# Kernel optimization log

Hardware: AMD Instinct MI355X
Metric: run time of the kernel (lower is better)

The kernel has to match this reference:

```python
import jax, jax.numpy as jnp
import numpy as np

ALPHA = 0.2          # LeakyReLU negative slope
NEG_INF = -9e15      # mask fill value used by the original module


def setup_inputs() -> dict:
    key = jax.random.key(0)
    k1, k2, k3, k4 = jax.random.split(key, 4)
    N, F_in, F_out = 8192, 256, 64
    h = jax.random.normal(k1, (N, F_in), dtype=jnp.float32)
    adj = jax.random.randint(k2, (N, N), 0, 2).astype(jnp.int32)
    # xavier_uniform with gain=1.414
    gain = 1.414
    bW = gain * np.sqrt(6.0 / (F_in + F_out))
    W = jax.random.uniform(k3, (F_in, F_out), dtype=jnp.float32, minval=-bW, maxval=bW)
    ba = gain * np.sqrt(6.0 / (2 * F_out + 1))
    a = jax.random.uniform(k4, (2 * F_out, 1), dtype=jnp.float32, minval=-ba, maxval=ba)
    return {"h": h, "adj": adj, "W": W, "a": a}


def reference(h, adj, W, a):
    # Wh: [N, F_out]
    Wh = h @ W
    F_out = Wh.shape[1]
    # Decompose a_input @ a: e[i, j] = leakyrelu(Wh[j]@a[:F] + Wh[i]@a[F:])
    # (repeat gives Wh[j] in the first half, repeat_interleave gives Wh[i] in the second)
    f_src = (Wh @ a[:F_out]).reshape(-1)   # [N], coefficient of column index j
    f_dst = (Wh @ a[F_out:]).reshape(-1)   # [N], coefficient of row index i
    e = jax.nn.leaky_relu(f_dst[:, None] + f_src[None, :], negative_slope=ALPHA)  # [N, N]
    attention = jnp.where(adj > 0, e, NEG_INF)
    attention = jax.nn.softmax(attention, axis=1)
    # dropout is identity in eval mode (training=False)
    h_prime = attention @ Wh               # [N, F_out]
    return jax.nn.elu(h_prime)             # concat=True path
```

## Files before the change

### kernel.cpp

```cpp
#include <hip/hip_runtime.h>
#include <hip/hip_bf16.h>

#define GN     8192
#define FIN    256
#define FOUT   64
#define NSPLIT 8
#define JSEG   1024
#define NCH    32
#define GRP    4
#define ROWS_B 128
#define LOG2E  1.44269504f

typedef float  f32x4  __attribute__((ext_vector_type(4)));
typedef __bf16 bf16x8 __attribute__((ext_vector_type(8)));
typedef int    iv4    __attribute__((ext_vector_type(4)));

__device__ __forceinline__ unsigned short f2bf_rtne(float x) {
    unsigned int u = __float_as_uint(x);
    unsigned int r = (u + 0x7FFFu + ((u >> 16) & 1u)) >> 16;
    return (unsigned short)r;
}

__global__ __launch_bounds__(256) void k_wh(const float* __restrict__ h,
                                            const float* __restrict__ W,
                                            const float* __restrict__ a,
                                            float* __restrict__ fsrc,
                                            float* __restrict__ fdst,
                                            uint4* __restrict__ whfrag) {
    __shared__ float Wt[FOUT][FIN + 1];
    __shared__ float WhL[32][FOUT + 1];
    int t = threadIdx.x;
    int col = t & 63, kq4 = t >> 6;
#pragma unroll
    for (int rep = 0; rep < 16; ++rep) {
        int k0 = kq4 * 4 + rep * 16;
        float4 wv;
        wv.x = W[(k0 + 0) * FOUT + col];
        wv.y = W[(k0 + 1) * FOUT + col];
        wv.z = W[(k0 + 2) * FOUT + col];
        wv.w = W[(k0 + 3) * FOUT + col];
        *(float4*)&Wt[col][k0] = wv;
    }
    __syncthreads();
    int wave = t >> 6, lane = t & 63;
    float a1 = a[lane], a2 = a[FOUT + lane];
    int bid = blockIdx.x;
#pragma unroll
    for (int rr = 0; rr < 8; ++rr) {
        int il = wave * 8 + rr;
        int i  = bid * 32 + il;
        const float* hrow = h + (size_t)i * FIN;
        float acc = 0.f;
#pragma unroll 8
        for (int k0 = 0; k0 < FIN; k0 += 4) {
            float4 hv = *(const float4*)&hrow[k0];
            float4 wv = *(const float4*)&Wt[lane][k0];
            acc += hv.x * wv.x + hv.y * wv.y + hv.z * wv.z + hv.w * wv.w;
        }
        WhL[il][lane] = acc;
        float v1 = acc * a1, v2 = acc * a2;
#pragma unroll
        for (int off = 32; off > 0; off >>= 1) {
            v1 += __shfl_xor(v1, off);
            v2 += __shfl_xor(v2, off);
        }
        if (lane == 0) {
            fsrc[i] = fminf(v1, 30.f) * LOG2E;
            fdst[i] = fminf(v2, 30.f) * LOG2E;
        }
    }
    __syncthreads();
    int lane2 = t & 63, ct = t >> 6;
    int colc = ct * 16 + (lane2 & 15);
    int gb = lane2 >> 4;
    unsigned int pk[4];
#pragma unroll
    for (int p = 0; p < 4; ++p) {
        int jo = ((p >> 1) * 16) + gb * 4 + (p & 1) * 2;
        unsigned int lo = f2bf_rtne(WhL[jo    ][colc]);
        unsigned int hi = f2bf_rtne(WhL[jo + 1][colc]);
        pk[p] = lo | (hi << 16);
    }
    uint4 o; o.x = pk[0]; o.y = pk[1]; o.z = pk[2]; o.w = pk[3];
    whfrag[(size_t)(bid * 4 + ct) * 64 + lane2] = o;
}

__global__ __launch_bounds__(512, 2) void k_attn(const int* __restrict__ adj,
                                                 const float* __restrict__ fsrc,
                                                 const float* __restrict__ fdst,
                                                 const uint4* __restrict__ whfrag,
                                                 float* __restrict__ pacc,
                                                 float* __restrict__ pden) {
    __shared__ uint4 whL[NCH * 4 * 64];
    __shared__ float fsL[JSEG];
    __shared__ unsigned bbuf[8][2][16][4];

    int t = threadIdx.x, wv = t >> 6, lane = t & 63;
    int bid = blockIdx.x;
    int rt = bid >> 3, q = bid & (NSPLIT - 1);
    int rowbase = rt * ROWS_B;
    int r = lane & 15, g = lane >> 4;
    int row16 = rowbase + wv * 16;

    const int* abase = adj + (size_t)row16 * GN + q * JSEG;
    iv4 st[16];
#pragma unroll
    for (int k = 0; k < 16; ++k)
        st[k] = *(const iv4*)(abase + (size_t)k * GN + lane * 4);

    {
        const uint4* src = whfrag + (size_t)q * (NCH * 4 * 64);
#pragma unroll
        for (int it = 0; it < 16; ++it) whL[it * 512 + t] = src[it * 512 + t];
        if (t < 256) *(float4*)&fsL[t * 4] = *(const float4*)&fsrc[q * JSEG + t * 4];
    }
    __syncthreads();

    float d = fdst[row16 + r];
    f32x4 acc0 = {0.f, 0.f, 0.f, 0.f}, acc1 = acc0, acc2 = acc0, acc3 = acc0;
    float den = 0.f;

    for (int grp = 0; grp < GRP; ++grp) {
#pragma unroll
        for (int k = 0; k < 16; ++k) {
            iv4 v = st[k];
            unsigned long long b0 = __ballot(v[0] > 0);
            unsigned long long b1 = __ballot(v[1] > 0);
            unsigned long long b2 = __ballot(v[2] > 0);
            unsigned long long b3 = __ballot(v[3] > 0);
            if (lane < 8) {
                unsigned long long s01 = (lane & 1) ? b1 : b0;
                unsigned long long s23 = (lane & 1) ? b3 : b2;
                unsigned long long ss  = (lane & 2) ? s23 : s01;
                bbuf[wv][lane >> 2][k][lane & 3] = (unsigned)(ss >> ((lane >> 2) * 32));
            }
        }
        if (grp + 1 < GRP) {
#pragma unroll
            for (int k = 0; k < 16; ++k)
                st[k] = *(const iv4*)(abase + (size_t)k * GN + (grp + 1) * 256 + lane * 4);
        }
#pragma unroll 4
        for (int chl = 0; chl < 8; ++chl) {
            int ch = grp * 8 + chl;
            uint4 W4 = *(const uint4*)&bbuf[wv][chl >> 2][r][0];
            float4 s0 = *(const float4*)&fsL[ch * 32 + g * 4];
            float4 s1 = *(const float4*)&fsL[ch * 32 + 16 + g * 4];
            const uint4* bl = &whL[(ch * 4) * 64 + lane];
            uint4 b0 = bl[0], b1 = bl[64], b2 = bl[128], b3 = bl[192];
            unsigned wc[4] = {W4.x, W4.y, W4.z, W4.w};
            float se[8] = {s0.x, s0.y, s0.z, s0.w, s1.x, s1.y, s1.z, s1.w};
            int sb = (chl & 3) * 8 + g;
            bf16x8 af;
            float ws = 0.f;
#pragma unroll
            for (int e = 0; e < 8; ++e) {
                float ev = d + se[e];
                float lr = fmaxf(ev, 0.2f * ev);
                float ex = __builtin_amdgcn_exp2f(lr);
                unsigned bit = (wc[e & 3] >> (sb + (e >> 2) * 4)) & 1u;
                float wvv = bit ? ex : 0.f;
                ws += wvv;
                af[e] = (__bf16)wvv;
            }
            den += ws;
            acc0 = __builtin_amdgcn_mfma_f32_16x16x32_bf16(af, __builtin_bit_cast(bf16x8, b0), acc0, 0, 0, 0);
            acc1 = __builtin_amdgcn_mfma_f32_16x16x32_bf16(af, __builtin_bit_cast(bf16x8, b1), acc1, 0, 0, 0);
            acc2 = __builtin_amdgcn_mfma_f32_16x16x32_bf16(af, __builtin_bit_cast(bf16x8, b2), acc2, 0, 0, 0);
            acc3 = __builtin_amdgcn_mfma_f32_16x16x32_bf16(af, __builtin_bit_cast(bf16x8, b3), acc3, 0, 0, 0);
        }
    }

    den += __shfl_xor(den, 16);
    den += __shfl_xor(den, 32);

    float* po = pacc + (size_t)q * (GN * FOUT);
    int orow = rowbase + wv * 16 + g * 4;
#pragma unroll
    for (int reg = 0; reg < 4; ++reg) {
        po[(size_t)(orow + reg) * FOUT +  0 + r] = acc0[reg];
        po[(size_t)(orow + reg) * FOUT + 16 + r] = acc1[reg];
        po[(size_t)(orow + reg) * FOUT + 32 + r] = acc2[reg];
        po[(size_t)(orow + reg) * FOUT + 48 + r] = acc3[reg];
    }
    if (g == 0) pden[(size_t)q * GN + row16 + r] = den;
}

__global__ __launch_bounds__(256) void k_out(const float* __restrict__ pacc,
                                             const float* __restrict__ pden,
                                             float* __restrict__ out) {
    int idx = blockIdx.x * 256 + threadIdx.x;
    int i = idx >> 6;
    float num = 0.f, den = 0.f;
#pragma unroll
    for (int qq = 0; qq < NSPLIT; ++qq) {
        num += pacc[(size_t)qq * (GN * FOUT) + idx];
        den += pden[(size_t)qq * GN + i];
    }
    float v = (den != 0.f) ? num / den : 0.f;
    out[idx] = v > 0.f ? v : __expf(v) - 1.f;
}

extern "C" void kernel_launch(void* const* d_in, const int* in_sizes, int n_in,
                              void* d_out, int out_size, void* d_ws, size_t ws_size,
                              hipStream_t stream) {
    (void)in_sizes; (void)n_in; (void)out_size; (void)ws_size;
    const float* h   = (const float*)d_in[0];
    const int*   adj = (const int*)d_in[1];
    const float* W   = (const float*)d_in[2];
    const float* a   = (const float*)d_in[3];
    float* out = (float*)d_out;

    float* ws     = (float*)d_ws;
    float* fsrc   = ws;
    float* fdst   = fsrc + GN;
    uint4* whfrag = (uint4*)(fdst + GN);
    float* pacc   = (float*)(whfrag + (size_t)GN / 32 * 4 * 64);
    float* pden   = pacc + (size_t)NSPLIT * GN * FOUT;

    k_wh  <<<GN / 32,                 256, 0, stream>>>(h, W, a, fsrc, fdst, whfrag);
    k_attn<<<(GN / ROWS_B) * NSPLIT,  512, 0, stream>>>(adj, fsrc, fdst, whfrag, pacc, pden);
    k_out <<<GN * FOUT / 256,         256, 0, stream>>>(pacc, pden, out);
}
```

Measured before the change: 111.9 us.

## Pack adjacency into bitmask in separate streaming kernel before attention

Adds a k_pack kernel that reads the full int32 adjacency matrix with nontemporal loads, several in flight at once, and writes a compact per-row bitmask. The attention kernel then loads its mask bits straight into registers instead of ballot-packing adj through shared memory interleaved with the MFMA work. The adjacency read moves into a dedicated streaming pass, and the attention kernel loses its LDS staging and barrier-free ballot stage. The cost is an extra launch and a small bitmask write and read through global memory.

New measurement: 122.5 us. 9.5% more time.

```diff
diff --git a/kernel.cpp b/kernel.cpp
--- a/kernel.cpp
+++ b/kernel.cpp
@@ -7,7 +7,6 @@
 #define NSPLIT 8
 #define JSEG   1024
 #define NCH    32
-#define GRP    4
 #define ROWS_B 128
 #define LOG2E  1.44269504f
 
@@ -19,6 +18,34 @@
     unsigned int u = __float_as_uint(x);
     unsigned int r = (u + 0x7FFFu + ((u >> 16) & 1u)) >> 16;
     return (unsigned short)r;
+}
+
+__global__ __launch_bounds__(256) void k_pack(const int* __restrict__ adj,
+                                              unsigned* __restrict__ bmask) {
+    int wv = threadIdx.x >> 6, lane = threadIdx.x & 63;
+    int row = blockIdx.x * 4 + wv;
+    const int* rp = adj + (size_t)row * GN;
+    iv4 st[4];
+#pragma unroll
+    for (int dd = 0; dd < 4; ++dd)
+        st[dd] = __builtin_nontemporal_load((const iv4*)(rp + dd * 256 + lane * 4));
+#pragma unroll 4
+    for (int gg = 0; gg < 32; ++gg) {
+        iv4 v = st[gg & 3];
+        unsigned long long b0 = __ballot(v[0] > 0);
+        unsigned long long b1 = __ballot(v[1] > 0);
+        unsigned long long b2 = __ballot(v[2] > 0);
+        unsigned long long b3 = __ballot(v[3] > 0);
+        int ng = gg + 4;
+        if (ng < 32)
+            st[gg & 3] = __builtin_nontemporal_load((const iv4*)(rp + ng * 256 + lane * 4));
+        if (lane < 8) {
+            unsigned long long s01 = (lane & 1) ? b1 : b0;
+            unsigned long long s23 = (lane & 1) ? b3 : b2;
+            unsigned long long ss  = (lane & 2) ? s23 : s01;
+            bmask[(size_t)row * 256 + gg * 8 + lane] = (unsigned)(ss >> ((lane >> 2) * 32));
+        }
+    }
 }
 
 __global__ __launch_bounds__(256) void k_wh(const float* __restrict__ h,
@@ -85,7 +112,7 @@
     whfrag[(size_t)(bid * 4 + ct) * 64 + lane2] = o;
 }
 
-__global__ __launch_bounds__(512, 2) void k_attn(const int* __restrict__ adj,
+__global__ __launch_bounds__(512, 2) void k_attn(const unsigned* __restrict__ bmask,
                                                  const float* __restrict__ fsrc,
                                                  const float* __restrict__ fdst,
                                                  const uint4* __restrict__ whfrag,
@@ -93,20 +120,19 @@
                                                  float* __restrict__ pden) {
     __shared__ uint4 whL[NCH * 4 * 64];
     __shared__ float fsL[JSEG];
-    __shared__ unsigned bbuf[8][2][16][4];
 
     int t = threadIdx.x, wv = t >> 6, lane = t & 63;
     int bid = blockIdx.x;
     int rt = bid >> 3, q = bid & (NSPLIT - 1);
     int rowbase = rt * ROWS_B;
     int r = lane & 15, g = lane >> 4;
-    int row16 = rowbase + wv * 16;
-
-    const int* abase = adj + (size_t)row16 * GN + q * JSEG;
-    iv4 st[16];
-#pragma unroll
-    for (int k = 0; k < 16; ++k)
-        st[k] = *(const iv4*)(abase + (size_t)k * GN + lane * 4);
+    int row = rowbase + wv * 16 + r;
+
+    const uint4* bm4 = (const uint4*)bmask + (size_t)row * 64 + q * 8;
+    uint4 M[8];
+#pragma unroll
+    for (int i = 0; i < 8; ++i) M[i] = bm4[i];
+    float d = fdst[row];
 
     {
         const uint4* src = whfrag + (size_t)q * (NCH * 4 * 64);
@@ -116,34 +142,15 @@
     }
     __syncthreads();
 
-    float d = fdst[row16 + r];
     f32x4 acc0 = {0.f, 0.f, 0.f, 0.f}, acc1 = acc0, acc2 = acc0, acc3 = acc0;
     float den = 0.f;
 
-    for (int grp = 0; grp < GRP; ++grp) {
-#pragma unroll
-        for (int k = 0; k < 16; ++k) {
-            iv4 v = st[k];
-            unsigned long long b0 = __ballot(v[0] > 0);
-            unsigned long long b1 = __ballot(v[1] > 0);
-            unsigned long long b2 = __ballot(v[2] > 0);
-            unsigned long long b3 = __ballot(v[3] > 0);
-            if (lane < 8) {
-                unsigned long long s01 = (lane & 1) ? b1 : b0;
-                unsigned long long s23 = (lane & 1) ? b3 : b2;
-                unsigned long long ss  = (lane & 2) ? s23 : s01;
-                bbuf[wv][lane >> 2][k][lane & 3] = (unsigned)(ss >> ((lane >> 2) * 32));
-            }
-        }
-        if (grp + 1 < GRP) {
-#pragma unroll
-            for (int k = 0; k < 16; ++k)
-                st[k] = *(const iv4*)(abase + (size_t)k * GN + (grp + 1) * 256 + lane * 4);
-        }
-#pragma unroll 4
+#pragma unroll
+    for (int grp = 0; grp < 4; ++grp) {
+#pragma unroll
         for (int chl = 0; chl < 8; ++chl) {
             int ch = grp * 8 + chl;
-            uint4 W4 = *(const uint4*)&bbuf[wv][chl >> 2][r][0];
+            uint4 W4 = M[grp * 2 + (chl >> 2)];
             float4 s0 = *(const float4*)&fsL[ch * 32 + g * 4];
             float4 s1 = *(const float4*)&fsL[ch * 32 + 16 + g * 4];
             const uint4* bl = &whL[(ch * 4) * 64 + lane];
@@ -183,7 +190,7 @@
         po[(size_t)(orow + reg) * FOUT + 32 + r] = acc2[reg];
         po[(size_t)(orow + reg) * FOUT + 48 + r] = acc3[reg];
     }
-    if (g == 0) pden[(size_t)q * GN + row16 + r] = den;
+    if (g == 0) pden[(size_t)q * GN + row] = den;
 }
 
 __global__ __launch_bounds__(256) void k_out(const float* __restrict__ pacc,
@@ -211,14 +218,16 @@
     const float* a   = (const float*)d_in[3];
     float* out = (float*)d_out;
 
-    float* ws     = (float*)d_ws;
-    float* fsrc   = ws;
-    float* fdst   = fsrc + GN;
-    uint4* whfrag = (uint4*)(fdst + GN);
-    float* pacc   = (float*)(whfrag + (size_t)GN / 32 * 4 * 64);
-    float* pden   = pacc + (size_t)NSPLIT * GN * FOUT;
-
+    float* ws       = (float*)d_ws;
+    float* fsrc     = ws;
+    float* fdst     = fsrc + GN;
+    uint4* whfrag   = (uint4*)(fdst + GN);
+    float* pacc     = (float*)(whfrag + (size_t)GN / 32 * 4 * 64);
+    float* pden     = pacc + (size_t)NSPLIT * GN * FOUT;
+    unsigned* bmask = (unsigned*)(pden + (size_t)NSPLIT * GN);
+
+    k_pack<<<GN / 4,                  256, 0, stream>>>(adj, bmask);
     k_wh  <<<GN / 32,                 256, 0, stream>>>(h, W, a, fsrc, fdst, whfrag);
-    k_attn<<<(GN / ROWS_B) * NSPLIT,  512, 0, stream>>>(adj, fsrc, fdst, whfrag, pacc, pden);
+    k_attn<<<(GN / ROWS_B) * NSPLIT,  512, 0, stream>>>(bmask, fsrc, fdst, whfrag, pacc, pden);
     k_out <<<GN * FOUT / 256,         256, 0, stream>>>(pacc, pden, out);
 }
```
